# Performance work log

Hardware: AMD Instinct MI355X
Metric: run time of the kernel (lower is better)

Reference implementation:

```python
import jax, jax.numpy as jnp
import numpy as np

B, T, D, H, V = 32, 64, 1024, 1024, 32000
MXLEN = 100
GO = 1  # Offsets.GO


def setup_inputs() -> dict:
    key = jax.random.key(0)
    k0, k1, k2, k3, k4 = jax.random.split(key, 5)
    return {
        "tgt": jax.random.randint(k0, (B, T), 0, V),
        "Wo": jax.random.normal(k1, (V, D), jnp.float32) * 0.02,      # tgt embedding / GreedyEmbeddingHelper table
        "Wx": jax.random.normal(k2, (D, 4 * H), jnp.float32) * (1.0 / np.sqrt(D)),
        "Wh": jax.random.normal(k3, (H, 4 * H), jnp.float32) * (1.0 / np.sqrt(H)),
        "b": jnp.zeros((4 * H,), jnp.float32),
        "Wp": jax.random.normal(k4, (H, V), jnp.float32) * 0.02,      # Dense(vsz, use_bias=False)
    }


def _lstm_step(h, c, x, Wx, Wh, b):
    z = x @ Wx + h @ Wh + b                      # [B, 4H]
    i, f, g, o = jnp.split(z, 4, axis=-1)
    c = jax.nn.sigmoid(f + 1.0) * c + jax.nn.sigmoid(i) * jnp.tanh(g)  # forget_bias=1.0 (TF LSTMCell)
    h = jax.nn.sigmoid(o) * jnp.tanh(c)
    return h, c


def reference(tgt, Wo, Wx, Wh, b, Wp):
    # --- teacher-forced decode (TrainingHelper + BasicDecoder) ---
    xs = jnp.swapaxes(Wo[tgt], 0, 1)             # [T, B, D] time-major
    h0 = jnp.zeros((B, H), Wo.dtype)
    c0 = jnp.zeros((B, H), Wo.dtype)

    def tf_step(carry, x):
        h, c = carry
        h, c = _lstm_step(h, c, x, Wx, Wh, b)
        return (h, c), h

    _, hs = jax.lax.scan(tf_step, (h0, c0), xs)  # [T, B, H]
    logits = jnp.einsum('tbh,hv->tbv', hs, Wp)   # self.preds, [T, B, V]
    probs = jax.nn.softmax(logits, axis=-1)      # DecoderBase.output softmax (beam==1)

    # --- greedy decode (GreedyEmbeddingHelper) ---
    tok0 = jnp.full((B,), GO, dtype=tgt.dtype)

    def greedy_step(carry, _):
        h, c, tok = carry
        x = Wo[tok]                              # feed back argmax embedding
        h, c = _lstm_step(h, c, x, Wx, Wh, b)
        lg = h @ Wp                              # [B, V]
        tok = jnp.argmax(lg, axis=-1)
        return (h, c, tok), tok

    _, best = jax.lax.scan(greedy_step, (h0, c0, tok0), None, length=MXLEN)  # [MXLEN, B]
    return logits, probs, best
```

## Files before the change

### kernel.cpp

```cpp
#include <hip/hip_runtime.h>

namespace {

constexpr int Bb = 32, Tt = 64, Dd = 1024, Hh = 1024, Vv = 32000, MX = 100;
constexpr long TBV = (long)Tt * Bb * Vv;

typedef __bf16 bf16x8 __attribute__((ext_vector_type(8)));
typedef float floatx4 __attribute__((ext_vector_type(4)));

__device__ __forceinline__ float sigf(float x) { return 1.0f / (1.0f + expf(-x)); }

__device__ __forceinline__ __bf16 f2bf(float x) {
  unsigned u = __builtin_bit_cast(unsigned, x);
  unsigned short r = (unsigned short)((u + 0x7FFFu + ((u >> 16) & 1u)) >> 16);
  return __builtin_bit_cast(__bf16, r);
}

__global__ __launch_bounds__(64) void init_tok(int* __restrict__ tok) {
  int i = threadIdx.x;
  if (i < Bb) tok[i] = 1;
}

__global__ __launch_bounds__(256) void gather_cast_x(
    const int* __restrict__ tgt, const float* __restrict__ Wo,
    __bf16* __restrict__ X) {
  int i = blockIdx.x * 256 + threadIdx.x;
  int row = i >> 7, ko = (i & 127) * 8;
  int tt = row >> 5, b = row & 31;
  const float* src = Wo + (long)tgt[b * Tt + tt] * Dd + ko;
  float4 v0 = *(const float4*)src, v1 = *(const float4*)(src + 4);
  bf16x8 w;
  w[0] = f2bf(v0.x); w[1] = f2bf(v0.y); w[2] = f2bf(v0.z); w[3] = f2bf(v0.w);
  w[4] = f2bf(v1.x); w[5] = f2bf(v1.y); w[6] = f2bf(v1.z); w[7] = f2bf(v1.w);
  *(bf16x8*)(X + (long)row * Dd + ko) = w;
}

__global__ __launch_bounds__(256) void transpose_cast(
    const float* __restrict__ in, __bf16* __restrict__ out, int K, int N) {
  __shared__ __bf16 tile[64][72];
  int k0 = blockIdx.y * 64, n0 = blockIdx.x * 64;
  int t = threadIdx.x;
#pragma unroll
  for (int cc = 0; cc < 4; cc++) {
    int cid = t + cc * 256;
    int kk = cid >> 4, nn = (cid & 15) * 4;
    float4 v = *(const float4*)(in + (long)(k0 + kk) * N + n0 + nn);
    tile[nn + 0][kk] = f2bf(v.x);
    tile[nn + 1][kk] = f2bf(v.y);
    tile[nn + 2][kk] = f2bf(v.z);
    tile[nn + 3][kk] = f2bf(v.w);
  }
  __syncthreads();
#pragma unroll
  for (int cc = 0; cc < 2; cc++) {
    int cid = t + cc * 256;
    int nn = cid >> 3, kk = (cid & 7) * 8;
    bf16x8 w;
#pragma unroll
    for (int j = 0; j < 8; j++) w[j] = tile[nn][kk + j];
    *(bf16x8*)(out + (long)(n0 + nn) * K + k0 + kk) = w;
  }
}

__global__ __launch_bounds__(256) void gemm_mfma(
    const __bf16* __restrict__ A, const __bf16* __restrict__ BT,
    float* __restrict__ C, int ldc, int K, const float* __restrict__ bias) {
  __shared__ __bf16 As[128 * 40];
  __shared__ __bf16 Bs[128 * 40];
  const int t = threadIdx.x;
  const int lane = t & 63, wave = t >> 6;
  const int m0 = blockIdx.y * 128, n0 = blockIdx.x * 128;
  const int wm = (wave >> 1) * 64, wn = (wave & 1) * 64;
  const int fr = lane & 15;
  const int fk = (lane >> 4) * 8;
  floatx4 acc[4][4] = {};
  for (int k0 = 0; k0 < K; k0 += 32) {
#pragma unroll
    for (int cc = 0; cc < 2; cc++) {
      int cid = t + cc * 256;
      int row = cid >> 2, ko = (cid & 3) * 8;
      *(bf16x8*)(As + row * 40 + ko) =
          *(const bf16x8*)(A + (long)(m0 + row) * K + k0 + ko);
      *(bf16x8*)(Bs + row * 40 + ko) =
          *(const bf16x8*)(BT + (long)(n0 + row) * K + k0 + ko);
    }
    __syncthreads();
    bf16x8 af[4], bg[4];
#pragma unroll
    for (int i = 0; i < 4; i++) {
      af[i] = *(const bf16x8*)(As + (wm + i * 16 + fr) * 40 + fk);
      bg[i] = *(const bf16x8*)(Bs + (wn + i * 16 + fr) * 40 + fk);
    }
#pragma unroll
    for (int i = 0; i < 4; i++)
#pragma unroll
      for (int j = 0; j < 4; j++)
        acc[i][j] = __builtin_amdgcn_mfma_f32_16x16x32_bf16(af[i], bg[j],
                                                            acc[i][j], 0, 0, 0);
    __syncthreads();
  }
  const int cr = (lane >> 4) * 4;
#pragma unroll
  for (int i = 0; i < 4; i++)
#pragma unroll
    for (int j = 0; j < 4; j++) {
      int n = n0 + wn + j * 16 + fr;
      float bv = bias ? bias[n] : 0.f;
#pragma unroll
      for (int r = 0; r < 4; r++) {
        int m = m0 + wm + i * 16 + cr + r;
        C[(long)m * ldc + n] = acc[i][j][r] + bv;
      }
    }
}

__global__ __launch_bounds__(256) void zpartA(
    const float* __restrict__ h, const float* __restrict__ Wh,
    float* __restrict__ zp) {
  __shared__ float As[32][33];
  __shared__ float Bs[32][64];
  const int t = threadIdx.x;
  const int n0 = blockIdx.x * 64, ks = blockIdx.y, kbase = ks * 256;
  const int lm = t & 31, kq = (t >> 5) * 4;
  const int bn = t & 63, kr = (t >> 6) * 8;
  const int mg = (t >> 5) * 4, ng = (t & 31) * 2;
  float acc[4][2] = {};
  for (int k0 = 0; k0 < 256; k0 += 32) {
    float4 av = *(const float4*)(h + (long)lm * Hh + kbase + k0 + kq);
    As[kq + 0][lm] = av.x; As[kq + 1][lm] = av.y;
    As[kq + 2][lm] = av.z; As[kq + 3][lm] = av.w;
    const float* Bp = Wh + (long)(kbase + k0 + kr) * 4096 + n0 + bn;
#pragma unroll
    for (int r = 0; r < 8; r++) Bs[kr + r][bn] = Bp[(long)r * 4096];
    __syncthreads();
#pragma unroll
    for (int k = 0; k < 32; k++) {
      float a0 = As[k][mg], a1 = As[k][mg + 1], a2 = As[k][mg + 2], a3 = As[k][mg + 3];
      float b0 = Bs[k][ng], b1 = Bs[k][ng + 1];
      acc[0][0] += a0 * b0; acc[0][1] += a0 * b1;
      acc[1][0] += a1 * b0; acc[1][1] += a1 * b1;
      acc[2][0] += a2 * b0; acc[2][1] += a2 * b1;
      acc[3][0] += a3 * b0; acc[3][1] += a3 * b1;
    }
    __syncthreads();
  }
#pragma unroll
  for (int i = 0; i < 4; i++)
#pragma unroll
    for (int j = 0; j < 2; j++)
      zp[((long)ks * 32 + mg + i) * 4096 + n0 + ng + j] = acc[i][j];
}

__global__ __launch_bounds__(256) void zpartB(
    const int* __restrict__ tok, const float* __restrict__ Wo,
    const float* __restrict__ Wx, const float* __restrict__ h,
    const float* __restrict__ Wh, float* __restrict__ zp) {
  __shared__ float As[32][33];
  __shared__ float Bs[32][64];
  __shared__ int stok[32];
  const int t = threadIdx.x;
  const int n0 = blockIdx.x * 64, ks = blockIdx.y;
  if (t < 32) stok[t] = tok[t];
  const int lm = t & 31, kq = (t >> 5) * 4;
  const int bn = t & 63, kr = (t >> 6) * 8;
  const int mg = (t >> 5) * 4, ng = (t & 31) * 2;
  float acc[4][2] = {};
  __syncthreads();
  const float* Arow;
  const float* Bsrc;
  int kbase;
  if (ks < 4) {
    kbase = ks * 256;
    Bsrc = Wx;
    Arow = Wo + (long)stok[lm] * Dd + kbase;
  } else {
    kbase = (ks - 4) * 256;
    Bsrc = Wh;
    Arow = h + (long)lm * Hh + kbase;
  }
  for (int k0 = 0; k0 < 256; k0 += 32) {
    float4 av = *(const float4*)(Arow + k0 + kq);
    As[kq + 0][lm] = av.x; As[kq + 1][lm] = av.y;
    As[kq + 2][lm] = av.z; As[kq + 3][lm] = av.w;
    const float* Bp = Bsrc + (long)(kbase + k0 + kr) * 4096 + n0 + bn;
#pragma unroll
    for (int r = 0; r < 8; r++) Bs[kr + r][bn] = Bp[(long)r * 4096];
    __syncthreads();
#pragma unroll
    for (int k = 0; k < 32; k++) {
      float a0 = As[k][mg], a1 = As[k][mg + 1], a2 = As[k][mg + 2], a3 = As[k][mg + 3];
      float b0 = Bs[k][ng], b1 = Bs[k][ng + 1];
      acc[0][0] += a0 * b0; acc[0][1] += a0 * b1;
      acc[1][0] += a1 * b0; acc[1][1] += a1 * b1;
      acc[2][0] += a2 * b0; acc[2][1] += a2 * b1;
      acc[3][0] += a3 * b0; acc[3][1] += a3 * b1;
    }
    __syncthreads();
  }
#pragma unroll
  for (int i = 0; i < 4; i++)
#pragma unroll
    for (int j = 0; j < 2; j++)
      zp[((long)ks * 32 + mg + i) * 4096 + n0 + ng + j] = acc[i][j];
}

__global__ __launch_bounds__(256) void gatesA(
    const float* __restrict__ base, const float* __restrict__ zp,
    float* __restrict__ h, float* __restrict__ c, __bf16* __restrict__ hsb) {
  int idx = blockIdx.x * 256 + threadIdx.x;
  int m = idx >> 10, n = idx & 1023;
  long o = (long)m * 4096 + n;
  float z[4];
#pragma unroll
  for (int g = 0; g < 4; g++) {
    float v = base[o + g * 1024];
#pragma unroll
    for (int ks = 0; ks < 4; ks++) v += zp[(long)ks * 131072 + o + g * 1024];
    z[g] = v;
  }
  float cn = sigf(z[1] + 1.0f) * c[idx] + sigf(z[0]) * tanhf(z[2]);
  float hn = sigf(z[3]) * tanhf(cn);
  c[idx] = cn;
  h[idx] = hn;
  hsb[idx] = f2bf(hn);
}

__global__ __launch_bounds__(256) void gatesB(
    const float* __restrict__ zp, const float* __restrict__ bias,
    float* __restrict__ h, float* __restrict__ c) {
  int idx = blockIdx.x * 256 + threadIdx.x;
  int m = idx >> 10, n = idx & 1023;
  long o = (long)m * 4096 + n;
  float z[4];
#pragma unroll
  for (int g = 0; g < 4; g++) {
    float v = bias[g * 1024 + n];
#pragma unroll
    for (int ks = 0; ks < 8; ks++) v += zp[(long)ks * 131072 + o + g * 1024];
    z[g] = v;
  }
  float cn = sigf(z[1] + 1.0f) * c[idx] + sigf(z[0]) * tanhf(z[2]);
  float hn = sigf(z[3]) * tanhf(cn);
  c[idx] = cn;
  h[idx] = hn;
}

__global__ __launch_bounds__(256) void lg_argmax_part(
    const float* __restrict__ h, const float* __restrict__ Wp,
    float* __restrict__ pv, int* __restrict__ pi) {
  __shared__ float As[32][33];
  __shared__ float Bs[32][64];
  __shared__ float rv[32][33];
  __shared__ int ri[32][33];
  const int t = threadIdx.x;
  const int n0 = blockIdx.x * 64;
  const int lm = t & 31, kq = (t >> 5) * 4;
  const int bn = t & 63, kr = (t >> 6) * 8;
  const int mg = (t >> 5) * 4, ng = (t & 31) * 2;
  float acc[4][2] = {};
  for (int k0 = 0; k0 < 1024; k0 += 32) {
    float4 av = *(const float4*)(h + (long)lm * Hh + k0 + kq);
    As[kq + 0][lm] = av.x; As[kq + 1][lm] = av.y;
    As[kq + 2][lm] = av.z; As[kq + 3][lm] = av.w;
    const float* Bp = Wp + (long)(k0 + kr) * Vv + n0 + bn;
#pragma unroll
    for (int r = 0; r < 8; r++) Bs[kr + r][bn] = Bp[(long)r * Vv];
    __syncthreads();
#pragma unroll
    for (int k = 0; k < 32; k++) {
      float a0 = As[k][mg], a1 = As[k][mg + 1], a2 = As[k][mg + 2], a3 = As[k][mg + 3];
      float b0 = Bs[k][ng], b1 = Bs[k][ng + 1];
      acc[0][0] += a0 * b0; acc[0][1] += a0 * b1;
      acc[1][0] += a1 * b0; acc[1][1] += a1 * b1;
      acc[2][0] += a2 * b0; acc[2][1] += a2 * b1;
      acc[3][0] += a3 * b0; acc[3][1] += a3 * b1;
    }
    __syncthreads();
  }
#pragma unroll
  for (int i = 0; i < 4; i++) {
    float v0 = acc[i][0], v1 = acc[i][1];
    int c0 = n0 + ng;
    float bvv = (v1 > v0) ? v1 : v0;
    int bii = (v1 > v0) ? (c0 + 1) : c0;
    rv[mg + i][t & 31] = bvv;
    ri[mg + i][t & 31] = bii;
  }
  __syncthreads();
  if (t < 32) {
    float bvv = -3.402823466e38f;
    int bii = 0x7fffffff;
    for (int j = 0; j < 32; j++) {
      float v = rv[t][j];
      int id = ri[t][j];
      if (v > bvv || (v == bvv && id < bii)) { bvv = v; bii = id; }
    }
    pv[t * 500 + blockIdx.x] = bvv;
    pi[t * 500 + blockIdx.x] = bii;
  }
}

__global__ __launch_bounds__(256) void argmax_fin(
    const float* __restrict__ pv, const int* __restrict__ pi,
    int* __restrict__ tok, float* __restrict__ best) {
  __shared__ float sv[256];
  __shared__ int si[256];
  int row = blockIdx.x, t = threadIdx.x;
  float bvv = -3.402823466e38f;
  int bii = 0x7fffffff;
  for (int j = t; j < 500; j += 256) {
    float v = pv[row * 500 + j];
    int id = pi[row * 500 + j];
    if (v > bvv || (v == bvv && id < bii)) { bvv = v; bii = id; }
  }
  sv[t] = bvv; si[t] = bii;
  __syncthreads();
  for (int s = 128; s > 0; s >>= 1) {
    if (t < s) {
      float v = sv[t + s]; int id = si[t + s];
      if (v > sv[t] || (v == sv[t] && id < si[t])) { sv[t] = v; si[t] = id; }
    }
    __syncthreads();
  }
  if (t == 0) { tok[row] = si[0]; best[row] = (float)si[0]; }
}

__global__ __launch_bounds__(256) void softmax_k(
    const float* __restrict__ lgts, float* __restrict__ pr) {
  __shared__ float rm[256], rs[256];
  const int r = blockIdx.x, t = threadIdx.x;
  const float* x = lgts + (long)r * Vv;
  float* p = pr + (long)r * Vv;
  float mx = -3.402823466e38f, sm = 0.f;
  for (int i = t; i < Vv; i += 256) {
    float v = x[i];
    if (v > mx) { sm = sm * __expf(mx - v) + 1.f; mx = v; }
    else sm += __expf(v - mx);
  }
  rm[t] = mx; rs[t] = sm;
  __syncthreads();
  for (int s = 128; s > 0; s >>= 1) {
    if (t < s) {
      float m2 = rm[t + s], s2 = rs[t + s];
      float M = fmaxf(rm[t], m2);
      rs[t] = rs[t] * __expf(rm[t] - M) + s2 * __expf(m2 - M);
      rm[t] = M;
    }
    __syncthreads();
  }
  float M = rm[0], inv = 1.f / rs[0];
  for (int i = t; i < Vv; i += 256) p[i] = __expf(x[i] - M) * inv;
}

}

extern "C" void kernel_launch(void* const* d_in, const int* in_sizes, int n_in,
                              void* d_out, int out_size, void* d_ws, size_t ws_size,
                              hipStream_t stream) {
  const int* tgt  = (const int*)d_in[0];
  const float* Wo = (const float*)d_in[1];
  const float* Wx = (const float*)d_in[2];
  const float* Wh = (const float*)d_in[3];
  const float* bb = (const float*)d_in[4];
  const float* Wp = (const float*)d_in[5];

  float* out = (float*)d_out;
  float* logits = out;
  float* probs = out + TBV;
  float* best = out + 2 * TBV;

  float* XZ = probs;
  __bf16* Xtm   = (__bf16*)(probs + 8388608);
  __bf16* hs_bf = (__bf16*)(probs + 8388608 + 1048576);
  __bf16* WxT   = (__bf16*)(probs + 8388608 + 2 * 1048576);
  __bf16* WpT   = (__bf16*)(probs + 8388608 + 4 * 1048576);

  float* ws = (float*)d_ws;
  float* h = ws;
  float* c = h + Bb * Hh;
  float* zp = c + Bb * Hh;
  float* pv = zp + 8 * Bb * 4 * Hh;
  int* pi = (int*)(pv + 32 * 500);
  int* tok = pi + 32 * 500;

  gather_cast_x<<<1024, 256, 0, stream>>>(tgt, Wo, Xtm);
  transpose_cast<<<dim3(64, 16), 256, 0, stream>>>(Wx, WxT, Dd, 4 * Hh);
  transpose_cast<<<dim3(500, 16), 256, 0, stream>>>(Wp, WpT, Hh, Vv);

  hipMemsetAsync(h, 0, 2 * Bb * Hh * sizeof(float), stream);
  gemm_mfma<<<dim3(32, 16), 256, 0, stream>>>(Xtm, WxT, XZ, 4 * Hh, Dd, bb);
  for (int t = 0; t < Tt; t++) {
    zpartA<<<dim3(64, 4), 256, 0, stream>>>(h, Wh, zp);
    gatesA<<<128, 256, 0, stream>>>(XZ + (long)t * Bb * 4 * Hh, zp, h, c,
                                    hs_bf + (long)t * Bb * Hh);
  }
  gemm_mfma<<<dim3(250, 16), 256, 0, stream>>>(hs_bf, WpT, logits, Vv, Hh,
                                               nullptr);

  hipMemsetAsync(h, 0, 2 * Bb * Hh * sizeof(float), stream);
  init_tok<<<1, 64, 0, stream>>>(tok);
  for (int s = 0; s < MX; s++) {
    zpartB<<<dim3(64, 8), 256, 0, stream>>>(tok, Wo, Wx, h, Wh, zp);
    gatesB<<<128, 256, 0, stream>>>(zp, bb, h, c);
    lg_argmax_part<<<500, 256, 0, stream>>>(h, Wp, pv, pi);
    argmax_fin<<<32, 256, 0, stream>>>(pv, pi, tok, best + s * Bb);
  }

  softmax_k<<<Tt * Bb, 256, 0, stream>>>(logits, probs);
}
```

Baseline: 11.56 ms.

## Fuse recurrent LSTM loops into persistent kernels with atomic grid barriers

The per-timestep kernel launches for the teacher-forced and greedy LSTM loops are replaced by two persistent kernels, 256 and 512 blocks. These loop over the steps internally and use atomic-counter grid barriers between the GEMM, gate, logits/argmax and final argmax phases. The shared GEMM tile routine is rewritten with register prefetch of the next K slice, float4 shared-memory loads and a 2x4 per-thread microtile. This removes hundreds of launch overheads. The risks are deadlock if not all blocks are co-resident, barrier latency, and idle blocks during the small phases.

```diff
diff --git a/kernel.cpp b/kernel.cpp
--- a/kernel.cpp
+++ b/kernel.cpp
@@ -114,215 +114,223 @@
     }
 }
 
-__global__ __launch_bounds__(256) void zpartA(
-    const float* __restrict__ h, const float* __restrict__ Wh,
-    float* __restrict__ zp) {
-  __shared__ float As[32][33];
-  __shared__ float Bs[32][64];
-  const int t = threadIdx.x;
-  const int n0 = blockIdx.x * 64, ks = blockIdx.y, kbase = ks * 256;
-  const int lm = t & 31, kq = (t >> 5) * 4;
-  const int bn = t & 63, kr = (t >> 6) * 8;
-  const int mg = (t >> 5) * 4, ng = (t & 31) * 2;
-  float acc[4][2] = {};
-  for (int k0 = 0; k0 < 256; k0 += 32) {
-    float4 av = *(const float4*)(h + (long)lm * Hh + kbase + k0 + kq);
-    As[kq + 0][lm] = av.x; As[kq + 1][lm] = av.y;
-    As[kq + 2][lm] = av.z; As[kq + 3][lm] = av.w;
-    const float* Bp = Wh + (long)(kbase + k0 + kr) * 4096 + n0 + bn;
-#pragma unroll
-    for (int r = 0; r < 8; r++) Bs[kr + r][bn] = Bp[(long)r * 4096];
+__device__ __forceinline__ void gridbar(int* __restrict__ ctr, int nblk) {
+  __syncthreads();
+  if (threadIdx.x == 0) {
+    __threadfence();
+    __hip_atomic_fetch_add(ctr, 1, __ATOMIC_RELEASE, __HIP_MEMORY_SCOPE_AGENT);
+    while (__hip_atomic_load(ctr, __ATOMIC_RELAXED, __HIP_MEMORY_SCOPE_AGENT) <
+           nblk)
+      __builtin_amdgcn_s_sleep(2);
+    __threadfence();
+  }
+  __syncthreads();
+}
+
+__device__ __forceinline__ void gemm_tile(float* __restrict__ Asm ,
+                                          float* __restrict__ Bsm ,
+                                          const float* __restrict__ Arow,
+                                          const float* __restrict__ Bt,
+                                          long ldb, int niter, int t,
+                                          float acc[2][4]) {
+  const int kq = (t >> 5) * 4, lm = t & 31;
+  const int kr = t >> 3, cb = (t & 7) * 8;
+  const int mg = (t >> 4) * 2, ng = (t & 15) * 4;
+  float4 av = *(const float4*)(Arow + kq);
+  float4 b0 = *(const float4*)Bt;
+  float4 b1 = *(const float4*)(Bt + 4);
+  for (int it = 0; it < niter; ++it) {
+    Asm[(kq + 0) * 34 + lm] = av.x;
+    Asm[(kq + 1) * 34 + lm] = av.y;
+    Asm[(kq + 2) * 34 + lm] = av.z;
+    Asm[(kq + 3) * 34 + lm] = av.w;
+    *(float4*)(&Bsm[kr * 64 + cb]) = b0;
+    *(float4*)(&Bsm[kr * 64 + cb + 4]) = b1;
     __syncthreads();
-#pragma unroll
-    for (int k = 0; k < 32; k++) {
-      float a0 = As[k][mg], a1 = As[k][mg + 1], a2 = As[k][mg + 2], a3 = As[k][mg + 3];
-      float b0 = Bs[k][ng], b1 = Bs[k][ng + 1];
-      acc[0][0] += a0 * b0; acc[0][1] += a0 * b1;
-      acc[1][0] += a1 * b0; acc[1][1] += a1 * b1;
-      acc[2][0] += a2 * b0; acc[2][1] += a2 * b1;
-      acc[3][0] += a3 * b0; acc[3][1] += a3 * b1;
+    if (it + 1 < niter) {
+      Arow += 32;
+      Bt += 32 * ldb;
+      av = *(const float4*)(Arow + kq);
+      b0 = *(const float4*)Bt;
+      b1 = *(const float4*)(Bt + 4);
+    }
+#pragma unroll
+    for (int k = 0; k < 32; ++k) {
+      float2 a = *(const float2*)(&Asm[k * 34 + mg]);
+      float4 bv = *(const float4*)(&Bsm[k * 64 + ng]);
+      acc[0][0] = fmaf(a.x, bv.x, acc[0][0]);
+      acc[0][1] = fmaf(a.x, bv.y, acc[0][1]);
+      acc[0][2] = fmaf(a.x, bv.z, acc[0][2]);
+      acc[0][3] = fmaf(a.x, bv.w, acc[0][3]);
+      acc[1][0] = fmaf(a.y, bv.x, acc[1][0]);
+      acc[1][1] = fmaf(a.y, bv.y, acc[1][1]);
+      acc[1][2] = fmaf(a.y, bv.z, acc[1][2]);
+      acc[1][3] = fmaf(a.y, bv.w, acc[1][3]);
     }
     __syncthreads();
   }
-#pragma unroll
-  for (int i = 0; i < 4; i++)
-#pragma unroll
-    for (int j = 0; j < 2; j++)
-      zp[((long)ks * 32 + mg + i) * 4096 + n0 + ng + j] = acc[i][j];
-}
-
-__global__ __launch_bounds__(256) void zpartB(
-    const int* __restrict__ tok, const float* __restrict__ Wo,
-    const float* __restrict__ Wx, const float* __restrict__ h,
-    const float* __restrict__ Wh, float* __restrict__ zp) {
-  __shared__ float As[32][33];
-  __shared__ float Bs[32][64];
-  __shared__ int stok[32];
-  const int t = threadIdx.x;
-  const int n0 = blockIdx.x * 64, ks = blockIdx.y;
-  if (t < 32) stok[t] = tok[t];
-  const int lm = t & 31, kq = (t >> 5) * 4;
-  const int bn = t & 63, kr = (t >> 6) * 8;
-  const int mg = (t >> 5) * 4, ng = (t & 31) * 2;
-  float acc[4][2] = {};
-  __syncthreads();
-  const float* Arow;
-  const float* Bsrc;
-  int kbase;
-  if (ks < 4) {
-    kbase = ks * 256;
-    Bsrc = Wx;
-    Arow = Wo + (long)stok[lm] * Dd + kbase;
-  } else {
-    kbase = (ks - 4) * 256;
-    Bsrc = Wh;
-    Arow = h + (long)lm * Hh + kbase;
-  }
-  for (int k0 = 0; k0 < 256; k0 += 32) {
-    float4 av = *(const float4*)(Arow + k0 + kq);
-    As[kq + 0][lm] = av.x; As[kq + 1][lm] = av.y;
-    As[kq + 2][lm] = av.z; As[kq + 3][lm] = av.w;
-    const float* Bp = Bsrc + (long)(kbase + k0 + kr) * 4096 + n0 + bn;
-#pragma unroll
-    for (int r = 0; r < 8; r++) Bs[kr + r][bn] = Bp[(long)r * 4096];
-    __syncthreads();
-#pragma unroll
-    for (int k = 0; k < 32; k++) {
-      float a0 = As[k][mg], a1 = As[k][mg + 1], a2 = As[k][mg + 2], a3 = As[k][mg + 3];
-      float b0 = Bs[k][ng], b1 = Bs[k][ng + 1];
-      acc[0][0] += a0 * b0; acc[0][1] += a0 * b1;
-      acc[1][0] += a1 * b0; acc[1][1] += a1 * b1;
-      acc[2][0] += a2 * b0; acc[2][1] += a2 * b1;
-      acc[3][0] += a3 * b0; acc[3][1] += a3 * b1;
-    }
-    __syncthreads();
-  }
-#pragma unroll
-  for (int i = 0; i < 4; i++)
-#pragma unroll
-    for (int j = 0; j < 2; j++)
-      zp[((long)ks * 32 + mg + i) * 4096 + n0 + ng + j] = acc[i][j];
-}
-
-__global__ __launch_bounds__(256) void gatesA(
-    const float* __restrict__ base, const float* __restrict__ zp,
-    float* __restrict__ h, float* __restrict__ c, __bf16* __restrict__ hsb) {
-  int idx = blockIdx.x * 256 + threadIdx.x;
-  int m = idx >> 10, n = idx & 1023;
-  long o = (long)m * 4096 + n;
-  float z[4];
-#pragma unroll
-  for (int g = 0; g < 4; g++) {
-    float v = base[o + g * 1024];
-#pragma unroll
-    for (int ks = 0; ks < 4; ks++) v += zp[(long)ks * 131072 + o + g * 1024];
-    z[g] = v;
-  }
-  float cn = sigf(z[1] + 1.0f) * c[idx] + sigf(z[0]) * tanhf(z[2]);
-  float hn = sigf(z[3]) * tanhf(cn);
-  c[idx] = cn;
-  h[idx] = hn;
-  hsb[idx] = f2bf(hn);
-}
-
-__global__ __launch_bounds__(256) void gatesB(
-    const float* __restrict__ zp, const float* __restrict__ bias,
-    float* __restrict__ h, float* __restrict__ c) {
-  int idx = blockIdx.x * 256 + threadIdx.x;
-  int m = idx >> 10, n = idx & 1023;
-  long o = (long)m * 4096 + n;
-  float z[4];
-#pragma unroll
-  for (int g = 0; g < 4; g++) {
-    float v = bias[g * 1024 + n];
-#pragma unroll
-    for (int ks = 0; ks < 8; ks++) v += zp[(long)ks * 131072 + o + g * 1024];
-    z[g] = v;
-  }
-  float cn = sigf(z[1] + 1.0f) * c[idx] + sigf(z[0]) * tanhf(z[2]);
-  float hn = sigf(z[3]) * tanhf(cn);
-  c[idx] = cn;
-  h[idx] = hn;
-}
-
-__global__ __launch_bounds__(256) void lg_argmax_part(
-    const float* __restrict__ h, const float* __restrict__ Wp,
-    float* __restrict__ pv, int* __restrict__ pi) {
-  __shared__ float As[32][33];
-  __shared__ float Bs[32][64];
-  __shared__ float rv[32][33];
-  __shared__ int ri[32][33];
-  const int t = threadIdx.x;
-  const int n0 = blockIdx.x * 64;
-  const int lm = t & 31, kq = (t >> 5) * 4;
-  const int bn = t & 63, kr = (t >> 6) * 8;
-  const int mg = (t >> 5) * 4, ng = (t & 31) * 2;
-  float acc[4][2] = {};
-  for (int k0 = 0; k0 < 1024; k0 += 32) {
-    float4 av = *(const float4*)(h + (long)lm * Hh + k0 + kq);
-    As[kq + 0][lm] = av.x; As[kq + 1][lm] = av.y;
-    As[kq + 2][lm] = av.z; As[kq + 3][lm] = av.w;
-    const float* Bp = Wp + (long)(k0 + kr) * Vv + n0 + bn;
-#pragma unroll
-    for (int r = 0; r < 8; r++) Bs[kr + r][bn] = Bp[(long)r * Vv];
-    __syncthreads();
-#pragma unroll
-    for (int k = 0; k < 32; k++) {
-      float a0 = As[k][mg], a1 = As[k][mg + 1], a2 = As[k][mg + 2], a3 = As[k][mg + 3];
-      float b0 = Bs[k][ng], b1 = Bs[k][ng + 1];
-      acc[0][0] += a0 * b0; acc[0][1] += a0 * b1;
-      acc[1][0] += a1 * b0; acc[1][1] += a1 * b1;
-      acc[2][0] += a2 * b0; acc[2][1] += a2 * b1;
-      acc[3][0] += a3 * b0; acc[3][1] += a3 * b1;
-    }
-    __syncthreads();
-  }
-#pragma unroll
-  for (int i = 0; i < 4; i++) {
-    float v0 = acc[i][0], v1 = acc[i][1];
-    int c0 = n0 + ng;
-    float bvv = (v1 > v0) ? v1 : v0;
-    int bii = (v1 > v0) ? (c0 + 1) : c0;
-    rv[mg + i][t & 31] = bvv;
-    ri[mg + i][t & 31] = bii;
-  }
-  __syncthreads();
-  if (t < 32) {
-    float bvv = -3.402823466e38f;
-    int bii = 0x7fffffff;
-    for (int j = 0; j < 32; j++) {
-      float v = rv[t][j];
-      int id = ri[t][j];
-      if (v > bvv || (v == bvv && id < bii)) { bvv = v; bii = id; }
-    }
-    pv[t * 500 + blockIdx.x] = bvv;
-    pi[t * 500 + blockIdx.x] = bii;
-  }
-}
-
-__global__ __launch_bounds__(256) void argmax_fin(
-    const float* __restrict__ pv, const int* __restrict__ pi,
-    int* __restrict__ tok, float* __restrict__ best) {
-  __shared__ float sv[256];
-  __shared__ int si[256];
-  int row = blockIdx.x, t = threadIdx.x;
-  float bvv = -3.402823466e38f;
-  int bii = 0x7fffffff;
-  for (int j = t; j < 500; j += 256) {
-    float v = pv[row * 500 + j];
-    int id = pi[row * 500 + j];
-    if (v > bvv || (v == bvv && id < bii)) { bvv = v; bii = id; }
-  }
-  sv[t] = bvv; si[t] = bii;
-  __syncthreads();
-  for (int s = 128; s > 0; s >>= 1) {
-    if (t < s) {
-      float v = sv[t + s]; int id = si[t + s];
-      if (v > sv[t] || (v == sv[t] && id < si[t])) { sv[t] = v; si[t] = id; }
-    }
-    __syncthreads();
-  }
-  if (t == 0) { tok[row] = si[0]; best[row] = (float)si[0]; }
+}
+
+__global__ __launch_bounds__(256, 2) void phaseA_all(
+    const float* __restrict__ XZ, const float* __restrict__ Wh,
+    float* __restrict__ zp, float* __restrict__ h, float* __restrict__ c,
+    __bf16* __restrict__ hsb, int* __restrict__ barc) {
+  __shared__ float Asm[32 * 34];
+  __shared__ float Bsm[32 * 64];
+  const int b = blockIdx.x, t = threadIdx.x;
+  const int n0 = (b & 63) * 64, ks = b >> 6;
+  const int lm = t & 31, kr = t >> 3, cb = (t & 7) * 8;
+  const int mg = (t >> 4) * 2, ng = (t & 15) * 4;
+  for (int step = 0; step < Tt; ++step) {
+    {
+      const float* Arow = h + (long)lm * Hh + ks * 256;
+      const float* Bt = Wh + (long)(ks * 256 + kr) * 4096 + n0 + cb;
+      float acc[2][4] = {};
+      gemm_tile(Asm, Bsm, Arow, Bt, 4096, 8, t, acc);
+#pragma unroll
+      for (int i = 0; i < 2; i++) {
+        floatx4 v = {acc[i][0], acc[i][1], acc[i][2], acc[i][3]};
+        *(floatx4*)(&zp[((long)ks * 32 + mg + i) * 4096 + n0 + ng]) = v;
+      }
+    }
+    gridbar(barc + step * 2, 256);
+    if (t < 128) {
+      int idx = b * 128 + t;
+      int m = idx >> 10, n = idx & 1023;
+      long o = (long)m * 4096 + n;
+      const float* base = XZ + (long)step * 131072;
+      float z[4];
+#pragma unroll
+      for (int g = 0; g < 4; g++) {
+        float v = base[o + g * 1024];
+#pragma unroll
+        for (int kss = 0; kss < 4; kss++)
+          v += zp[(long)kss * 131072 + o + g * 1024];
+        z[g] = v;
+      }
+      float cn = sigf(z[1] + 1.0f) * c[idx] + sigf(z[0]) * tanhf(z[2]);
+      float hn = sigf(z[3]) * tanhf(cn);
+      c[idx] = cn;
+      h[idx] = hn;
+      hsb[(long)step * 32768 + idx] = f2bf(hn);
+    }
+    gridbar(barc + step * 2 + 1, 256);
+  }
+}
+
+__global__ __launch_bounds__(256, 2) void phaseB_all(
+    const float* __restrict__ Wo, const float* __restrict__ Wx,
+    const float* __restrict__ Wh, const float* __restrict__ bias,
+    const float* __restrict__ Wp, float* __restrict__ h, float* __restrict__ c,
+    float* __restrict__ zp, float* __restrict__ pv, int* __restrict__ pi,
+    int* __restrict__ tok, float* __restrict__ best, int* __restrict__ barc) {
+  __shared__ float Asm[32 * 34];
+  __shared__ float Bsm[32 * 64];
+  __shared__ float rv[32 * 16];
+  __shared__ int ri[32 * 16];
+  const int b = blockIdx.x, t = threadIdx.x;
+  const int lm = t & 31, kr = t >> 3, cb = (t & 7) * 8;
+  const int mg = (t >> 4) * 2, ng = (t & 15) * 4;
+  for (int s = 0; s < MX; ++s) {
+    int* bs = barc + s * 4;
+    {
+      const int n0 = (b & 63) * 64, ks = b >> 6;
+      const float* Arow;
+      const float* Bt;
+      if (ks < 4) {
+        int kbase = ks * 256;
+        Arow = Wo + (long)tok[lm] * Dd + kbase;
+        Bt = Wx + (long)(kbase + kr) * 4096 + n0 + cb;
+      } else {
+        int kbase = (ks - 4) * 256;
+        Arow = h + (long)lm * Hh + kbase;
+        Bt = Wh + (long)(kbase + kr) * 4096 + n0 + cb;
+      }
+      float acc[2][4] = {};
+      gemm_tile(Asm, Bsm, Arow, Bt, 4096, 8, t, acc);
+#pragma unroll
+      for (int i = 0; i < 2; i++) {
+        floatx4 v = {acc[i][0], acc[i][1], acc[i][2], acc[i][3]};
+        *(floatx4*)(&zp[((long)ks * 32 + mg + i) * 4096 + n0 + ng]) = v;
+      }
+    }
+    gridbar(bs + 0, 512);
+    if (t < 64) {
+      int idx = b * 64 + t;
+      int m = idx >> 10, n = idx & 1023;
+      long o = (long)m * 4096 + n;
+      float z[4];
+#pragma unroll
+      for (int g = 0; g < 4; g++) {
+        float v = bias[g * 1024 + n];
+#pragma unroll
+        for (int kss = 0; kss < 8; kss++)
+          v += zp[(long)kss * 131072 + o + g * 1024];
+        z[g] = v;
+      }
+      float cn = sigf(z[1] + 1.0f) * c[idx] + sigf(z[0]) * tanhf(z[2]);
+      float hn = sigf(z[3]) * tanhf(cn);
+      c[idx] = cn;
+      h[idx] = hn;
+    }
+    gridbar(bs + 1, 512);
+    if (b < 500) {
+      const int n0 = b * 64;
+      const float* Arow = h + (long)lm * Hh;
+      const float* Bt = Wp + (long)kr * Vv + n0 + cb;
+      float acc[2][4] = {};
+      gemm_tile(Asm, Bsm, Arow, Bt, Vv, 32, t, acc);
+      const int cbase = n0 + ng;
+#pragma unroll
+      for (int i = 0; i < 2; i++) {
+        float bvv = acc[i][0];
+        int bii = cbase;
+#pragma unroll
+        for (int j = 1; j < 4; j++)
+          if (acc[i][j] > bvv) { bvv = acc[i][j]; bii = cbase + j; }
+        rv[(mg + i) * 16 + (t & 15)] = bvv;
+        ri[(mg + i) * 16 + (t & 15)] = bii;
+      }
+      __syncthreads();
+      if (t < 32) {
+        float bvv = -3.402823466e38f;
+        int bii = 0x7fffffff;
+        for (int j = 0; j < 16; j++) {
+          float v = rv[t * 16 + j];
+          int id = ri[t * 16 + j];
+          if (v > bvv || (v == bvv && id < bii)) { bvv = v; bii = id; }
+        }
+        pv[t * 500 + b] = bvv;
+        pi[t * 500 + b] = bii;
+      }
+    }
+    gridbar(bs + 2, 512);
+    if (b == 0) {
+      int r = t >> 3, j = t & 7;
+      float bvv = -3.402823466e38f;
+      int bii = 0x7fffffff;
+      for (int e = j; e < 500; e += 8) {
+        float v = pv[r * 500 + e];
+        int id = pi[r * 500 + e];
+        if (v > bvv || (v == bvv && id < bii)) { bvv = v; bii = id; }
+      }
+      rv[r * 8 + j] = bvv;
+      ri[r * 8 + j] = bii;
+      __syncthreads();
+      if (t < 32) {
+        float fv = rv[t * 8];
+        int fi = ri[t * 8];
+        for (int j2 = 1; j2 < 8; j2++) {
+          float v = rv[t * 8 + j2];
+          int id = ri[t * 8 + j2];
+          if (v > fv || (v == fv && id < fi)) { fv = v; fi = id; }
+        }
+        tok[t] = fi;
+        best[s * Bb + t] = (float)fi;
+      }
+    }
+    gridbar(bs + 3, 512);
+  }
 }
 
 __global__ __launch_bounds__(256) void softmax_k(
@@ -382,29 +390,23 @@
   float* pv = zp + 8 * Bb * 4 * Hh;
   int* pi = (int*)(pv + 32 * 500);
   int* tok = pi + 32 * 500;
+  int* barc = tok + 32;
 
   gather_cast_x<<<1024, 256, 0, stream>>>(tgt, Wo, Xtm);
   transpose_cast<<<dim3(64, 16), 256, 0, stream>>>(Wx, WxT, Dd, 4 * Hh);
   transpose_cast<<<dim3(500, 16), 256, 0, stream>>>(Wp, WpT, Hh, Vv);
+  hipMemsetAsync(barc, 0, 1024 * sizeof(int), stream);
 
   hipMemsetAsync(h, 0, 2 * Bb * Hh * sizeof(float), stream);
   gemm_mfma<<<dim3(32, 16), 256, 0, stream>>>(Xtm, WxT, XZ, 4 * Hh, Dd, bb);
-  for (int t = 0; t < Tt; t++) {
-    zpartA<<<dim3(64, 4), 256, 0, stream>>>(h, Wh, zp);
-    gatesA<<<128, 256, 0, stream>>>(XZ + (long)t * Bb * 4 * Hh, zp, h, c,
-                                    hs_bf + (long)t * Bb * Hh);
-  }
+  phaseA_all<<<256, 256, 0, stream>>>(XZ, Wh, zp, h, c, hs_bf, barc);
   gemm_mfma<<<dim3(250, 16), 256, 0, stream>>>(hs_bf, WpT, logits, Vv, Hh,
                                                nullptr);
 
   hipMemsetAsync(h, 0, 2 * Bb * Hh * sizeof(float), stream);
   init_tok<<<1, 64, 0, stream>>>(tok);
-  for (int s = 0; s < MX; s++) {
-    zpartB<<<dim3(64, 8), 256, 0, stream>>>(tok, Wo, Wx, h, Wh, zp);
-    gatesB<<<128, 256, 0, stream>>>(zp, bb, h, c);
-    lg_argmax_part<<<500, 256, 0, stream>>>(h, Wp, pv, pi);
-    argmax_fin<<<32, 256, 0, stream>>>(pv, pi, tok, best + s * Bb);
-  }
+  phaseB_all<<<512, 256, 0, stream>>>(Wo, Wx, Wh, bb, Wp, h, c, zp, pv, pi,
+                                      tok, best, barc + 128);
 
   softmax_k<<<Tt * Bb, 256, 0, stream>>>(logits, probs);
 }
```

Result: slower. 32.03 ms (+177.0%).
